# Kernel tuning notes

Hardware: AMD Instinct MI355X
Metric: run time of the kernel (lower is better)

## Reference

```python
import jax, jax.numpy as jnp
import numpy as np

N = 50000   # num_entities
F = 300     # node feature dim
D = 128     # embedding_dim
H = 4       # heads
C = D // H  # per-head out channels (32)
E = 640000  # num edges
R = 200     # num_relations
L = 2       # num_layers
NEG_SLOPE = 0.2  # PyG GATv2Conv default


def setup_inputs() -> dict:
    key = jax.random.key(0)
    ks = jax.random.split(key, 14)
    s = 0.1
    return {
        "entity": jnp.arange(N, dtype=jnp.int32),
        "edge_index": jax.random.randint(ks[0], (2, E), 0, N, dtype=jnp.int32),
        "edge_type": jax.random.randint(ks[1], (E,), 0, R, dtype=jnp.int32),
        # learned parameters
        "node_features": jax.random.normal(ks[2], (N, F), jnp.float32) * s,   # entity_embedding table
        "rel_emb": jax.random.normal(ks[3], (R, D), jnp.float32) * s,          # relation_embedding
        "proj_w": jax.random.normal(ks[4], (F, D), jnp.float32) * s,           # project Linear
        "proj_b": jnp.zeros((D,), jnp.float32),
        # per-layer GATv2Conv params, stacked over L layers
        "w_l": jax.random.normal(ks[5], (L, D, H * C), jnp.float32) * s,       # lin_l weight
        "b_l": jnp.zeros((L, H * C), jnp.float32),
        "w_r": jax.random.normal(ks[6], (L, D, H * C), jnp.float32) * s,       # lin_r weight
        "b_r": jnp.zeros((L, H * C), jnp.float32),
        "w_e": jax.random.normal(ks[7], (L, D, H * C), jnp.float32) * s,       # lin_edge weight (no bias)
        "att": jax.random.normal(ks[8], (L, H, C), jnp.float32) * s,           # attention vector a
        "bias": jnp.zeros((L, H * C), jnp.float32),                             # output bias
    }


def _gatv2_layer(x, src, dst, edge_attr, w_l, b_l, w_r, b_r, w_e, att, bias):
    # x: [N, D], edge_attr: [E, D]
    x_l = (x @ w_l + b_l).reshape(N, H, C)
    x_r = (x @ w_r + b_r).reshape(N, H, C)
    e = (edge_attr @ w_e).reshape(E, H, C)
    # per-edge message (gather src/dst + edge), GATv2: leaky_relu BEFORE attention dot
    m = jax.nn.leaky_relu(x_l[src] + x_r[dst] + e, NEG_SLOPE)   # [E, H, C]
    logits = jnp.einsum('ehc,hc->eh', m, att)                    # [E, H]
    # segment softmax over edges grouped by destination node
    lmax = jax.ops.segment_max(logits, dst, num_segments=N)      # [N, H]
    ex = jnp.exp(logits - lmax[dst])                             # [E, H]
    denom = jax.ops.segment_sum(ex, dst, num_segments=N)         # [N, H]
    alpha = ex / denom[dst]                                      # [E, H]
    # scatter-aggregate messages x_l[src] weighted by alpha
    out = jax.ops.segment_sum(x_l[src] * alpha[:, :, None], dst, num_segments=N)  # [N, H, C]
    return out.reshape(N, H * C) + bias


def reference(entity, edge_index, edge_type, node_features, rel_emb,
              proj_w, proj_b, w_l, b_l, w_r, b_r, w_e, att, bias):
    x = node_features[entity]            # embedding lookup
    x = x @ proj_w + proj_b              # project to D
    edge_attr = rel_emb[edge_type]       # [E, D] (weights=False -> no edge_weight scaling)
    src, dst = edge_index[0], edge_index[1]
    for i in range(L):
        x = _gatv2_layer(x, src, dst, edge_attr,
                         w_l[i], b_l[i], w_r[i], b_r[i], w_e[i], att[i], bias[i])
        if i != L - 1:
            x = jax.nn.elu(x)            # dropout inactive (eval mode)
    return x
```

## Files before the change

kernel.cpp:

```cpp
#include <hip/hip_runtime.h>

#define NN 50000
#define FF 300
#define DD 128
#define HH 4
#define CC 32
#define EE 640000
#define RR 200
#define LL 2
#define SB ((NN + 255) / 256)
#define PK 320
#define WTOT (128 * PK + 4 * 128 * 128)
#define HB ((EE + 255) / 256)
#define WB ((WTOT + 255) / 256)
#define RB (LL * RR / 2)

typedef unsigned short u16;
typedef unsigned int u32;
typedef _Float16 h2   __attribute__((ext_vector_type(2)));
typedef _Float16 half8 __attribute__((ext_vector_type(8)));
typedef __attribute__((ext_vector_type(4))) float floatx4;

__device__ __forceinline__ u16 f2h(float f) {
    union { _Float16 h; u16 u; } v; v.h = (_Float16)f; return v.u;
}
__device__ __forceinline__ float h2f(u16 u) {
    union { u16 u; _Float16 h; } v; v.u = u; return (float)v.h;
}
__device__ __forceinline__ h2 u2h2(u32 p) {
    union { u32 u; h2 h; } v; v.u = p; return v.h;
}
__device__ __forceinline__ h2 hmax2(h2 a, h2 b) {
#if __has_builtin(__builtin_elementwise_max)
    return __builtin_elementwise_max(a, b);
#else
    h2 r; r.x = a.x > b.x ? a.x : b.x; r.y = a.y > b.y ? a.y : b.y; return r;
#endif
}
__device__ __forceinline__ float hdot2(h2 a, h2 b, float c) {
#if __has_builtin(__builtin_amdgcn_fdot2)
    return __builtin_amdgcn_fdot2(a, b, c, false);
#else
    return c + (float)a.x * (float)b.x + (float)a.y * (float)b.y;
#endif
}

__device__ __forceinline__ int block_excl_scan(int v, int* lds4, int* total) {
    int lane = threadIdx.x & 63, wid = threadIdx.x >> 6;
    int x = v;
    #pragma unroll
    for (int off = 1; off < 64; off <<= 1) {
        int y = __shfl_up(x, off, 64);
        if (lane >= off) x += y;
    }
    if (lane == 63) lds4[wid] = x;
    __syncthreads();
    int add = 0;
    #pragma unroll
    for (int w = 0; w < 4; w++) add += (w < wid) ? lds4[w] : 0;
    *total = lds4[0] + lds4[1] + lds4[2] + lds4[3];
    return x + add - v;
}

__global__ __launch_bounds__(256)
void prep_kernel(const int* __restrict__ ei, int* __restrict__ counts,
                 const float* __restrict__ proj_w, const float* __restrict__ w_l,
                 const float* __restrict__ w_r, u16* __restrict__ wt,
                 const float* __restrict__ rel_emb, const float* __restrict__ w_e,
                 u16* __restrict__ erel)
{
    __shared__ float rv[2][DD];
    int b = blockIdx.x, tid = threadIdx.x;
    if (b < HB) {
        int e = b * 256 + tid;
        if (e < EE) atomicAdd(&counts[ei[EE + e]], 1);
    } else if (b < HB + WB) {
        int i = (b - HB) * 256 + tid;
        if (i < WTOT) {
            float v;
            if (i < 128 * PK) {
                int n = i / PK, k = i - n * PK;
                v = (k < FF) ? proj_w[(size_t)k * DD + n] : 0.f;
            } else {
                int j = i - 128 * PK;
                int seg = j >> 14;
                int r = j & 16383;
                int n = r >> 7, k = r & 127;
                const float* src = (seg < 2) ? (w_l + (size_t)seg * DD * DD)
                                             : (w_r + (size_t)(seg - 2) * DD * DD);
                v = src[(size_t)k * DD + n];
            }
            wt[i] = f2h(v);
        }
    } else {
        int half = tid >> 7, d = tid & 127;
        int lr = (b - HB - WB) * 2 + half;
        int l = lr / RR, r = lr - l * RR;
        rv[half][d] = rel_emb[r * DD + d];
        __syncthreads();
        const float* W = w_e + (size_t)l * DD * DD;
        float acc = 0.f;
        #pragma unroll 8
        for (int k = 0; k < DD; k++) acc += rv[half][k] * W[k * DD + d];
        erel[(size_t)lr * DD + d] = f2h(acc);
    }
}

template<bool AF16, bool GATHER>
__global__ __launch_bounds__(256)
void gemm_mfma_kernel(const void* __restrict__ A_, const int* __restrict__ rowidx,
                      int lda, int K, int Ka, int ldb,
                      const u16* __restrict__ BT1, const float* __restrict__ bias1,
                      u16* __restrict__ C1,
                      const u16* __restrict__ BT2, const float* __restrict__ bias2,
                      u16* __restrict__ C2, int M)
{
    const u16*   BT   = (blockIdx.y == 0) ? BT1 : BT2;
    const float* bias = (blockIdx.y == 0) ? bias1 : bias2;
    u16*         Cout = (blockIdx.y == 0) ? C1 : C2;

    __shared__ u16 As[128][72];
    __shared__ u16 Bs[128][72];
    int tid  = threadIdx.x;
    int m0   = blockIdx.x * 128;
    int wave = tid >> 6, lane = tid & 63;
    int quad = lane >> 4, l16 = lane & 15;
    int wrow = (wave >> 1) * 64, wcol = (wave & 1) * 64;

    floatx4 acc[4][4];
    #pragma unroll
    for (int i = 0; i < 4; i++)
        #pragma unroll
        for (int j = 0; j < 4; j++) acc[i][j] = (floatx4){0.f, 0.f, 0.f, 0.f};

    int ar = tid >> 1, ah = tid & 1;
    int arow = m0 + ar;
    int rid = (arow < M) ? (GATHER ? rowidx[arow] : arow) : 0;

    for (int kk = 0; kk < K; kk += 64) {
        #pragma unroll
        for (int q = 0; q < 2; q++) {
            int kb = kk + ah * 32 + q * 16;
            u16 tmp[16];
            if (AF16) {
                const u16* Ap = (const u16*)A_ + (size_t)rid * lda + kb;
                if (kb + 16 <= Ka) {
                    *(half8*)&tmp[0] = *(const half8*)Ap;
                    *(half8*)&tmp[8] = *(const half8*)(Ap + 8);
                } else {
                    #pragma unroll
                    for (int j = 0; j < 16; j++) tmp[j] = (kb + j < Ka) ? Ap[j] : (u16)0;
                }
            } else {
                const float* Ap = (const float*)A_ + (size_t)rid * lda + kb;
                if (kb + 16 <= Ka) {
                    #pragma unroll
                    for (int qq = 0; qq < 4; qq++) {
                        float4 f = *(const float4*)(Ap + qq * 4);
                        tmp[qq*4+0] = f2h(f.x); tmp[qq*4+1] = f2h(f.y);
                        tmp[qq*4+2] = f2h(f.z); tmp[qq*4+3] = f2h(f.w);
                    }
                } else {
                    #pragma unroll
                    for (int j = 0; j < 16; j++) tmp[j] = (kb + j < Ka) ? f2h(Ap[j]) : (u16)0;
                }
            }
            *(half8*)&As[ar][ah * 32 + q * 16]     = *(half8*)&tmp[0];
            *(half8*)&As[ar][ah * 32 + q * 16 + 8] = *(half8*)&tmp[8];
        }
        {
            const u16* Bp = BT + (size_t)ar * ldb + kk + ah * 32;
            #pragma unroll
            for (int q = 0; q < 4; q++)
                *(half8*)&Bs[ar][ah * 32 + q * 8] = *(const half8*)(Bp + q * 8);
        }
        __syncthreads();
        #pragma unroll
        for (int ks = 0; ks < 2; ks++) {
            half8 af[4], bfr[4];
            #pragma unroll
            for (int i = 0; i < 4; i++)
                af[i] = *(const half8*)&As[wrow + i * 16 + l16][ks * 32 + quad * 8];
            #pragma unroll
            for (int j = 0; j < 4; j++)
                bfr[j] = *(const half8*)&Bs[wcol + j * 16 + l16][ks * 32 + quad * 8];
            #pragma unroll
            for (int i = 0; i < 4; i++)
                #pragma unroll
                for (int j = 0; j < 4; j++)
                    acc[i][j] = __builtin_amdgcn_mfma_f32_16x16x32_f16(
                        af[i], bfr[j], acc[i][j], 0, 0, 0);
        }
        __syncthreads();
    }

    #pragma unroll
    for (int i = 0; i < 4; i++) {
        #pragma unroll
        for (int rr = 0; rr < 4; rr++) {
            int row = m0 + wrow + i * 16 + quad * 4 + rr;
            if (row < M) {
                #pragma unroll
                for (int j = 0; j < 4; j++) {
                    int col = wcol + j * 16 + l16;
                    Cout[(size_t)row * DD + col] = f2h(acc[i][j][rr] + bias[col]);
                }
            }
        }
    }
}

__global__ __launch_bounds__(256)
void scan_local_kernel(const int* __restrict__ counts, int* __restrict__ offsets,
                       int* __restrict__ bsum)
{
    __shared__ int lds4[4];
    int i = blockIdx.x * 256 + threadIdx.x;
    int v = (i < NN) ? counts[i] : 0;
    int total;
    int ex = block_excl_scan(v, lds4, &total);
    if (i < NN) offsets[i] = ex;
    if (threadIdx.x == 0) bsum[blockIdx.x] = total;
}

__global__ __launch_bounds__(256)
void scan_bsum_kernel(int* __restrict__ bsum)
{
    __shared__ int lds4[4];
    int t = threadIdx.x;
    int v = (t < SB) ? bsum[t] : 0;
    int total;
    int ex = block_excl_scan(v, lds4, &total);
    if (t < SB) bsum[t] = ex;
}

__global__ __launch_bounds__(256)
void scatter_kernel(const int* __restrict__ ei, const int* __restrict__ et,
                    const int* __restrict__ offsets, const int* __restrict__ bsum,
                    int* __restrict__ fill, u32* __restrict__ dstorder)
{
    int e = blockIdx.x * 256 + threadIdx.x;
    if (e >= EE) return;
    int d = ei[EE + e];
    int pos = offsets[d] + bsum[d >> 8] + atomicAdd(&fill[d], 1);
    dstorder[pos] = (u32)ei[e] | ((u32)et[e] << 16);
}

__global__ __launch_bounds__(256)
void node_kernel(const u32* __restrict__ dstorder, const int* __restrict__ offsets,
                 const int* __restrict__ bsum,
                 const u16* __restrict__ xl, const u16* __restrict__ xr,
                 const u16* __restrict__ erel, const float* __restrict__ att,
                 const float* __restrict__ bias,
                 u16* __restrict__ xnext, float* __restrict__ outp, int is_last)
{
    int tid  = threadIdx.x;
    int node = blockIdx.x * 4 + (tid >> 6);
    int lane = tid & 63;
    if (node >= NN) return;
    int g  = lane >> 4;
    int gl = lane & 15;
    int c0 = gl * 8;
    int beg = offsets[node] + bsum[node >> 8];
    int end = (node == NN - 1) ? EE : offsets[node + 1] + bsum[(node + 1) >> 8];

    h2 xrh[4], atth[4];
    {
        const u32* xp = (const u32*)&xr[(size_t)node * DD + c0];
        #pragma unroll
        for (int q = 0; q < 4; q++) xrh[q] = u2h2(xp[q]);
        #pragma unroll
        for (int q = 0; q < 4; q++) {
            float2 av = *(const float2*)&att[c0 + q * 2];
            atth[q] = (h2){(_Float16)av.x, (_Float16)av.y};
        }
    }
    const h2 c02 = (h2){(_Float16)0.2f, (_Float16)0.2f};

    float s = 0.f;
    h2 a2[4];
    #pragma unroll
    for (int q = 0; q < 4; q++) a2[q] = (h2){(_Float16)0.f, (_Float16)0.f};

    for (int base = beg; base < end; base += 4) {
        int es = base + g;
        bool valid = es < end;
        u32 st = valid ? dstorder[es] : 0;
        int src = st & 0xffff;
        int typ = st >> 16;
        const u32* xp = (const u32*)&xl[(size_t)src * DD + c0];
        const u32* ep = (const u32*)&erel[(size_t)typ * DD + c0];
        h2 xh[4];
        float p = 0.f;
        #pragma unroll
        for (int q = 0; q < 4; q++) {
            xh[q] = u2h2(xp[q]);
            h2 m = (xh[q] + xrh[q]) + u2h2(ep[q]);
            m = hmax2(m, m * c02);
            p = hdot2(m, atth[q], p);
        }
        p += __shfl_xor(p, 1, 64);
        p += __shfl_xor(p, 2, 64);
        float w = valid ? __expf(fminf(p, 60.f)) : 0.f;
        s += w;
        h2 wh = (h2){(_Float16)w, (_Float16)w};
        #pragma unroll
        for (int q = 0; q < 4; q++) a2[q] += wh * xh[q];
    }

    float a[8];
    #pragma unroll
    for (int q = 0; q < 4; q++) { a[q*2] = (float)a2[q].x; a[q*2+1] = (float)a2[q].y; }
    #pragma unroll
    for (int j = 0; j < 8; j++) {
        a[j] += __shfl_xor(a[j], 16, 64);
        a[j] += __shfl_xor(a[j], 32, 64);
    }
    s += __shfl_xor(s, 16, 64);
    s += __shfl_xor(s, 32, 64);

    if (lane < 16) {
        float rh = 1.f / fmaxf(s, 1e-30f);
        float4 b0 = *(const float4*)&bias[c0];
        float4 b1 = *(const float4*)&bias[c0 + 4];
        float bv[8] = {b0.x, b0.y, b0.z, b0.w, b1.x, b1.y, b1.z, b1.w};
        float v[8];
        #pragma unroll
        for (int j = 0; j < 8; j++) v[j] = a[j] * rh + bv[j];
        if (is_last) {
            float4* op = (float4*)&outp[(size_t)node * DD + c0];
            op[0] = make_float4(v[0], v[1], v[2], v[3]);
            op[1] = make_float4(v[4], v[5], v[6], v[7]);
        } else {
            u16 pk[8];
            #pragma unroll
            for (int j = 0; j < 8; j++) {
                float w2 = v[j] > 0.f ? v[j] : __expf(v[j]) - 1.f;
                pk[j] = f2h(w2);
            }
            *(half8*)&xnext[(size_t)node * DD + c0] = *(half8*)pk;
        }
    }
}

extern "C" void kernel_launch(void* const* d_in, const int* in_sizes, int n_in,
                              void* d_out, int out_size, void* d_ws, size_t ws_size,
                              hipStream_t stream)
{
    const int*   entity        = (const int*)d_in[0];
    const int*   edge_index    = (const int*)d_in[1];
    const int*   edge_type     = (const int*)d_in[2];
    const float* node_features = (const float*)d_in[3];
    const float* rel_emb       = (const float*)d_in[4];
    const float* proj_w        = (const float*)d_in[5];
    const float* proj_b        = (const float*)d_in[6];
    const float* w_l           = (const float*)d_in[7];
    const float* b_l           = (const float*)d_in[8];
    const float* w_r           = (const float*)d_in[9];
    const float* b_r           = (const float*)d_in[10];
    const float* w_e           = (const float*)d_in[11];
    const float* att           = (const float*)d_in[12];
    const float* bias          = (const float*)d_in[13];

    u16*   xb      = (u16*)d_ws;
    u16*   xl      = xb + (size_t)NN * DD;
    u16*   xr      = xl + (size_t)NN * DD;
    u16*   erel    = xr + (size_t)NN * DD;
    u16*   wt      = erel + (size_t)LL * RR * DD;
    u32*   dstorder= (u32*)(wt + WTOT);
    int*   counts  = (int*)(dstorder + (size_t)EE);
    int*   fill    = counts + NN;
    int*   offsets = fill + NN;
    int*   bsum    = offsets + NN;

    hipMemsetAsync(counts, 0, (size_t)NN * 2 * sizeof(int), stream);
    prep_kernel<<<HB + WB + RB, 256, 0, stream>>>(
        edge_index, counts, proj_w, w_l, w_r, wt, rel_emb, w_e, erel);

    scan_local_kernel<<<SB, 256, 0, stream>>>(counts, offsets, bsum);
    scan_bsum_kernel<<<1, 256, 0, stream>>>(bsum);
    scatter_kernel<<<(EE + 255) / 256, 256, 0, stream>>>(
        edge_index, edge_type, offsets, bsum, fill, dstorder);

    const u16* wtProj = wt;
    const int GB = (NN + 127) / 128;
    gemm_mfma_kernel<false, true><<<dim3(GB, 1), 256, 0, stream>>>(
        node_features, entity, FF, PK, FF, PK,
        wtProj, proj_b, xb, wtProj, proj_b, xb, NN);

    for (int l = 0; l < LL; l++) {
        const u16* wtl = wt + 128 * PK + l * 16384;
        const u16* wtr = wt + 128 * PK + 32768 + l * 16384;
        gemm_mfma_kernel<true, false><<<dim3(GB, 2), 256, 0, stream>>>(
            xb, nullptr, DD, DD, DD, DD,
            wtl, b_l + l * DD, xl,
            wtr, b_r + l * DD, xr, NN);

        node_kernel<<<(NN + 3) / 4, 256, 0, stream>>>(
            dstorder, offsets, bsum, xl, xr, erel + (size_t)l * RR * DD,
            att + (size_t)l * DD, bias + (size_t)l * DD,
            xb, (float*)d_out, l == LL - 1);
    }
}
```

Before: 333.1 us.

## Fold projection into layer-0 weights, fuse dual GEMM, prefetch edges in node kernel

Layer-0 lin_l and lin_r are folded into the input projection by precomputing proj_w@w_l and proj_w@w_r, plus the matching fused biases, in the prep kernel. This removes one whole GEMM pass and the fp16 intermediate x. The GEMM now computes both outputs from a single 64-row A tile with a 256-column B tile, so A is read once instead of twice. The node kernel now uses 8 lanes per edge with 16 channels each, handles 8 edges per iteration, and software-prefetches the next edge's gathers. The risks are more fp16 rounding from the folded weights and extra registers in the node kernel.

```diff
diff --git a/kernel.cpp b/kernel.cpp
--- a/kernel.cpp
+++ b/kernel.cpp
@@ -10,9 +10,11 @@
 #define LL 2
 #define SB ((NN + 255) / 256)
 #define PK 320
-#define WTOT (128 * PK + 4 * 128 * 128)
+#define WCONV (2 * 128 * 128)
+#define WTOT (2 * 128 * PK + WCONV)
 #define HB ((EE + 255) / 256)
-#define WB ((WTOT + 255) / 256)
+#define WB (WCONV / 256)
+#define FB PK
 #define RB (LL * RR / 2)
 
 typedef unsigned short u16;
@@ -67,7 +69,9 @@
                  const float* __restrict__ proj_w, const float* __restrict__ w_l,
                  const float* __restrict__ w_r, u16* __restrict__ wt,
                  const float* __restrict__ rel_emb, const float* __restrict__ w_e,
-                 u16* __restrict__ erel)
+                 u16* __restrict__ erel, const float* __restrict__ proj_b,
+                 const float* __restrict__ b_l, const float* __restrict__ b_r,
+                 float* __restrict__ fbias)
 {
     __shared__ float rv[2][DD];
     int b = blockIdx.x, tid = threadIdx.x;
@@ -76,25 +80,36 @@
         if (e < EE) atomicAdd(&counts[ei[EE + e]], 1);
     } else if (b < HB + WB) {
         int i = (b - HB) * 256 + tid;
-        if (i < WTOT) {
-            float v;
-            if (i < 128 * PK) {
-                int n = i / PK, k = i - n * PK;
-                v = (k < FF) ? proj_w[(size_t)k * DD + n] : 0.f;
-            } else {
-                int j = i - 128 * PK;
-                int seg = j >> 14;
-                int r = j & 16383;
-                int n = r >> 7, k = r & 127;
-                const float* src = (seg < 2) ? (w_l + (size_t)seg * DD * DD)
-                                             : (w_r + (size_t)(seg - 2) * DD * DD);
-                v = src[(size_t)k * DD + n];
-            }
-            wt[i] = f2h(v);
-        }
+        int seg = i >> 14;
+        int r = i & 16383;
+        int n = r >> 7, k = r & 127;
+        const float* src = (seg == 0 ? w_l : w_r) + (size_t)DD * DD;
+        wt[2 * 128 * PK + i] = f2h(src[(size_t)k * DD + n]);
+    } else if (b < HB + WB + FB) {
+        int half = tid >> 7, d = tid & 127;
+        int pp = (b - HB - WB) * 2 + half;
+        int lr = pp / PK, k = pp - lr * PK;
+        rv[half][d] = (k < FF) ? proj_w[(size_t)k * DD + d] : 0.f;
+        __syncthreads();
+        float acc = 0.f;
+        if (k < FF) {
+            const float* W = lr ? w_r : w_l;
+            #pragma unroll 8
+            for (int j = 0; j < DD; j++) acc += rv[half][j] * W[(size_t)j * DD + d];
+        }
+        wt[(size_t)lr * 128 * PK + (size_t)d * PK + k] = f2h(acc);
+    } else if (b == HB + WB + FB) {
+        int half = tid >> 7, d = tid & 127;
+        if (tid < DD) rv[0][tid] = proj_b[tid];
+        __syncthreads();
+        const float* W = half ? w_r : w_l;
+        float acc = half ? b_r[d] : b_l[d];
+        #pragma unroll 8
+        for (int j = 0; j < DD; j++) acc += rv[0][j] * W[(size_t)j * DD + d];
+        fbias[half * DD + d] = acc;
     } else {
         int half = tid >> 7, d = tid & 127;
-        int lr = (b - HB - WB) * 2 + half;
+        int lr = (b - HB - WB - FB - 1) * 2 + half;
         int l = lr / RR, r = lr - l * RR;
         rv[half][d] = rel_emb[r * DD + d];
         __syncthreads();
@@ -108,24 +123,20 @@
 
 template<bool AF16, bool GATHER>
 __global__ __launch_bounds__(256)
-void gemm_mfma_kernel(const void* __restrict__ A_, const int* __restrict__ rowidx,
+void gemm_dual_kernel(const void* __restrict__ A_, const int* __restrict__ rowidx,
                       int lda, int K, int Ka, int ldb,
                       const u16* __restrict__ BT1, const float* __restrict__ bias1,
                       u16* __restrict__ C1,
                       const u16* __restrict__ BT2, const float* __restrict__ bias2,
                       u16* __restrict__ C2, int M)
 {
-    const u16*   BT   = (blockIdx.y == 0) ? BT1 : BT2;
-    const float* bias = (blockIdx.y == 0) ? bias1 : bias2;
-    u16*         Cout = (blockIdx.y == 0) ? C1 : C2;
-
-    __shared__ u16 As[128][72];
-    __shared__ u16 Bs[128][72];
+    __shared__ u16 As[64][72];
+    __shared__ u16 Bs[256][72];
     int tid  = threadIdx.x;
-    int m0   = blockIdx.x * 128;
+    int m0   = blockIdx.x * 64;
     int wave = tid >> 6, lane = tid & 63;
     int quad = lane >> 4, l16 = lane & 15;
-    int wrow = (wave >> 1) * 64, wcol = (wave & 1) * 64;
+    int wcol = wave * 64;
 
     floatx4 acc[4][4];
     #pragma unroll
@@ -133,77 +144,76 @@
         #pragma unroll
         for (int j = 0; j < 4; j++) acc[i][j] = (floatx4){0.f, 0.f, 0.f, 0.f};
 
-    int ar = tid >> 1, ah = tid & 1;
+    int ar = tid >> 2, ak = (tid & 3) * 16;
     int arow = m0 + ar;
     int rid = (arow < M) ? (GATHER ? rowidx[arow] : arow) : 0;
+    const u16* Brow = (tid < 128) ? (BT1 + (size_t)tid * ldb)
+                                  : (BT2 + (size_t)(tid - 128) * ldb);
 
     for (int kk = 0; kk < K; kk += 64) {
-        #pragma unroll
-        for (int q = 0; q < 2; q++) {
-            int kb = kk + ah * 32 + q * 16;
-            u16 tmp[16];
-            if (AF16) {
-                const u16* Ap = (const u16*)A_ + (size_t)rid * lda + kb;
-                if (kb + 16 <= Ka) {
-                    *(half8*)&tmp[0] = *(const half8*)Ap;
-                    *(half8*)&tmp[8] = *(const half8*)(Ap + 8);
-                } else {
-                    #pragma unroll
-                    for (int j = 0; j < 16; j++) tmp[j] = (kb + j < Ka) ? Ap[j] : (u16)0;
+        int kb = kk + ak;
+        u16 tmp[16];
+        if (AF16) {
+            const u16* Ap = (const u16*)A_ + (size_t)rid * lda + kb;
+            if (kb + 16 <= Ka) {
+                *(half8*)&tmp[0] = *(const half8*)Ap;
+                *(half8*)&tmp[8] = *(const half8*)(Ap + 8);
+            } else {
+                #pragma unroll
+                for (int j = 0; j < 16; j++) tmp[j] = (kb + j < Ka) ? Ap[j] : (u16)0;
+            }
+        } else {
+            const float* Ap = (const float*)A_ + (size_t)rid * lda + kb;
+            if (kb + 16 <= Ka) {
+                #pragma unroll
+                for (int qq = 0; qq < 4; qq++) {
+                    float4 f = *(const float4*)(Ap + qq * 4);
+                    tmp[qq*4+0] = f2h(f.x); tmp[qq*4+1] = f2h(f.y);
+                    tmp[qq*4+2] = f2h(f.z); tmp[qq*4+3] = f2h(f.w);
                 }
             } else {
-                const float* Ap = (const float*)A_ + (size_t)rid * lda + kb;
-                if (kb + 16 <= Ka) {
-                    #pragma unroll
-                    for (int qq = 0; qq < 4; qq++) {
-                        float4 f = *(const float4*)(Ap + qq * 4);
-                        tmp[qq*4+0] = f2h(f.x); tmp[qq*4+1] = f2h(f.y);
-                        tmp[qq*4+2] = f2h(f.z); tmp[qq*4+3] = f2h(f.w);
-                    }
-                } else {
-                    #pragma unroll
-                    for (int j = 0; j < 16; j++) tmp[j] = (kb + j < Ka) ? f2h(Ap[j]) : (u16)0;
-                }
+                #pragma unroll
+                for (int j = 0; j < 16; j++) tmp[j] = (kb + j < Ka) ? f2h(Ap[j]) : (u16)0;
             }
-            *(half8*)&As[ar][ah * 32 + q * 16]     = *(half8*)&tmp[0];
-            *(half8*)&As[ar][ah * 32 + q * 16 + 8] = *(half8*)&tmp[8];
-        }
-        {
-            const u16* Bp = BT + (size_t)ar * ldb + kk + ah * 32;
-            #pragma unroll
-            for (int q = 0; q < 4; q++)
-                *(half8*)&Bs[ar][ah * 32 + q * 8] = *(const half8*)(Bp + q * 8);
-        }
+        }
+        *(half8*)&As[ar][ak]     = *(half8*)&tmp[0];
+        *(half8*)&As[ar][ak + 8] = *(half8*)&tmp[8];
+        #pragma unroll
+        for (int q = 0; q < 8; q++)
+            *(half8*)&Bs[tid][q * 8] = *(const half8*)(Brow + kk + q * 8);
         __syncthreads();
         #pragma unroll
         for (int ks = 0; ks < 2; ks++) {
-            half8 af[4], bfr[4];
+            half8 af[4], bf[4];
             #pragma unroll
             for (int i = 0; i < 4; i++)
-                af[i] = *(const half8*)&As[wrow + i * 16 + l16][ks * 32 + quad * 8];
+                af[i] = *(const half8*)&As[i * 16 + l16][ks * 32 + quad * 8];
             #pragma unroll
             for (int j = 0; j < 4; j++)
-                bfr[j] = *(const half8*)&Bs[wcol + j * 16 + l16][ks * 32 + quad * 8];
+                bf[j] = *(const half8*)&Bs[wcol + j * 16 + l16][ks * 32 + quad * 8];
             #pragma unroll
             for (int i = 0; i < 4; i++)
                 #pragma unroll
                 for (int j = 0; j < 4; j++)
                     acc[i][j] = __builtin_amdgcn_mfma_f32_16x16x32_f16(
-                        af[i], bfr[j], acc[i][j], 0, 0, 0);
+                        af[i], bf[j], acc[i][j], 0, 0, 0);
         }
         __syncthreads();
     }
 
+    u16* Cw = (wave < 2) ? C1 : C2;
+    const float* bw = (wave < 2) ? bias1 : bias2;
+    int cbase = wcol & 127;
     #pragma unroll
     for (int i = 0; i < 4; i++) {
         #pragma unroll
         for (int rr = 0; rr < 4; rr++) {
-            int row = m0 + wrow + i * 16 + quad * 4 + rr;
+            int row = m0 + i * 16 + quad * 4 + rr;
             if (row < M) {
                 #pragma unroll
                 for (int j = 0; j < 4; j++) {
-                    int col = wcol + j * 16 + l16;
-                    Cout[(size_t)row * DD + col] = f2h(acc[i][j][rr] + bias[col]);
+                    int col = cbase + j * 16 + l16;
+                    Cw[(size_t)row * DD + col] = f2h(acc[i][j][rr] + bw[col]);
                 }
             }
         }
@@ -258,19 +268,19 @@
     int node = blockIdx.x * 4 + (tid >> 6);
     int lane = tid & 63;
     if (node >= NN) return;
-    int g  = lane >> 4;
-    int gl = lane & 15;
-    int c0 = gl * 8;
+    int g  = lane >> 3;
+    int gl = lane & 7;
+    int c0 = gl * 16;
     int beg = offsets[node] + bsum[node >> 8];
     int end = (node == NN - 1) ? EE : offsets[node + 1] + bsum[(node + 1) >> 8];
 
-    h2 xrh[4], atth[4];
+    h2 xrh[8], atth[8];
     {
         const u32* xp = (const u32*)&xr[(size_t)node * DD + c0];
         #pragma unroll
-        for (int q = 0; q < 4; q++) xrh[q] = u2h2(xp[q]);
-        #pragma unroll
-        for (int q = 0; q < 4; q++) {
+        for (int q = 0; q < 8; q++) xrh[q] = u2h2(xp[q]);
+        #pragma unroll
+        for (int q = 0; q < 8; q++) {
             float2 av = *(const float2*)&att[c0 + q * 2];
             atth[q] = (h2){(_Float16)av.x, (_Float16)av.y};
         }
@@ -278,67 +288,89 @@
     const h2 c02 = (h2){(_Float16)0.2f, (_Float16)0.2f};
 
     float s = 0.f;
-    h2 a2[4];
-    #pragma unroll
-    for (int q = 0; q < 4; q++) a2[q] = (h2){(_Float16)0.f, (_Float16)0.f};
-
-    for (int base = beg; base < end; base += 4) {
-        int es = base + g;
-        bool valid = es < end;
-        u32 st = valid ? dstorder[es] : 0;
-        int src = st & 0xffff;
-        int typ = st >> 16;
+    h2 a2[8];
+    #pragma unroll
+    for (int q = 0; q < 8; q++) a2[q] = (h2){(_Float16)0.f, (_Float16)0.f};
+
+    int es = beg + g;
+    u32 stB = (es + 8 < end) ? dstorder[es + 8] : 0u;
+    h2 xhA[8], ehA[8];
+    {
+        u32 stA = (es < end) ? dstorder[es] : 0u;
+        int src = stA & 0xffff, typ = stA >> 16;
         const u32* xp = (const u32*)&xl[(size_t)src * DD + c0];
         const u32* ep = (const u32*)&erel[(size_t)typ * DD + c0];
-        h2 xh[4];
+        #pragma unroll
+        for (int q = 0; q < 8; q++) { xhA[q] = u2h2(xp[q]); ehA[q] = u2h2(ep[q]); }
+    }
+
+    for (int base = beg; base < end; base += 8) {
+        u32 stN = (base + 16 + g < end) ? dstorder[base + 16 + g] : 0u;
+        h2 xhB[8], ehB[8];
+        {
+            int src = stB & 0xffff, typ = stB >> 16;
+            const u32* xp = (const u32*)&xl[(size_t)src * DD + c0];
+            const u32* ep = (const u32*)&erel[(size_t)typ * DD + c0];
+            #pragma unroll
+            for (int q = 0; q < 8; q++) { xhB[q] = u2h2(xp[q]); ehB[q] = u2h2(ep[q]); }
+        }
         float p = 0.f;
         #pragma unroll
-        for (int q = 0; q < 4; q++) {
-            xh[q] = u2h2(xp[q]);
-            h2 m = (xh[q] + xrh[q]) + u2h2(ep[q]);
+        for (int q = 0; q < 8; q++) {
+            h2 m = (xhA[q] + xrh[q]) + ehA[q];
             m = hmax2(m, m * c02);
             p = hdot2(m, atth[q], p);
         }
         p += __shfl_xor(p, 1, 64);
-        p += __shfl_xor(p, 2, 64);
+        bool valid = (base + g) < end;
         float w = valid ? __expf(fminf(p, 60.f)) : 0.f;
         s += w;
         h2 wh = (h2){(_Float16)w, (_Float16)w};
         #pragma unroll
-        for (int q = 0; q < 4; q++) a2[q] += wh * xh[q];
-    }
-
-    float a[8];
-    #pragma unroll
-    for (int q = 0; q < 4; q++) { a[q*2] = (float)a2[q].x; a[q*2+1] = (float)a2[q].y; }
-    #pragma unroll
-    for (int j = 0; j < 8; j++) {
+        for (int q = 0; q < 8; q++) a2[q] += wh * xhA[q];
+        #pragma unroll
+        for (int q = 0; q < 8; q++) { xhA[q] = xhB[q]; ehA[q] = ehB[q]; }
+        stB = stN;
+    }
+
+    float a[16];
+    #pragma unroll
+    for (int q = 0; q < 8; q++) { a[q*2] = (float)a2[q].x; a[q*2+1] = (float)a2[q].y; }
+    #pragma unroll
+    for (int j = 0; j < 16; j++) {
+        a[j] += __shfl_xor(a[j], 8, 64);
         a[j] += __shfl_xor(a[j], 16, 64);
         a[j] += __shfl_xor(a[j], 32, 64);
     }
+    s += __shfl_xor(s, 8, 64);
     s += __shfl_xor(s, 16, 64);
     s += __shfl_xor(s, 32, 64);
 
-    if (lane < 16) {
+    if (lane < 8) {
+        int cc = lane * 16;
         float rh = 1.f / fmaxf(s, 1e-30f);
-        float4 b0 = *(const float4*)&bias[c0];
-        float4 b1 = *(const float4*)&bias[c0 + 4];
-        float bv[8] = {b0.x, b0.y, b0.z, b0.w, b1.x, b1.y, b1.z, b1.w};
-        float v[8];
-        #pragma unroll
-        for (int j = 0; j < 8; j++) v[j] = a[j] * rh + bv[j];
+        float bv[16], v[16];
+        #pragma unroll
+        for (int qq = 0; qq < 4; qq++) {
+            float4 bq = *(const float4*)&bias[cc + qq * 4];
+            bv[qq*4+0] = bq.x; bv[qq*4+1] = bq.y; bv[qq*4+2] = bq.z; bv[qq*4+3] = bq.w;
+        }
+        #pragma unroll
+        for (int j = 0; j < 16; j++) v[j] = a[j] * rh + bv[j];
         if (is_last) {
-            float4* op = (float4*)&outp[(size_t)node * DD + c0];
-            op[0] = make_float4(v[0], v[1], v[2], v[3]);
-            op[1] = make_float4(v[4], v[5], v[6], v[7]);
+            float4* op = (float4*)&outp[(size_t)node * DD + cc];
+            #pragma unroll
+            for (int qq = 0; qq < 4; qq++)
+                op[qq] = make_float4(v[qq*4+0], v[qq*4+1], v[qq*4+2], v[qq*4+3]);
         } else {
-            u16 pk[8];
-            #pragma unroll
-            for (int j = 0; j < 8; j++) {
+            u16 pk[16];
+            #pragma unroll
+            for (int j = 0; j < 16; j++) {
                 float w2 = v[j] > 0.f ? v[j] : __expf(v[j]) - 1.f;
                 pk[j] = f2h(w2);
             }
-            *(half8*)&xnext[(size_t)node * DD + c0] = *(half8*)pk;
+            *(half8*)&xnext[(size_t)node * DD + cc]     = *(half8*)&pk[0];
+            *(half8*)&xnext[(size_t)node * DD + cc + 8] = *(half8*)&pk[8];
         }
     }
 }
@@ -372,33 +404,33 @@
     int*   fill    = counts + NN;
     int*   offsets = fill + NN;
     int*   bsum    = offsets + NN;
+    float* fbias   = (float*)(bsum + SB);
 
     hipMemsetAsync(counts, 0, (size_t)NN * 2 * sizeof(int), stream);
-    prep_kernel<<<HB + WB + RB, 256, 0, stream>>>(
-        edge_index, counts, proj_w, w_l, w_r, wt, rel_emb, w_e, erel);
+    prep_kernel<<<HB + WB + FB + 1 + RB, 256, 0, stream>>>(
+        edge_index, counts, proj_w, w_l, w_r, wt, rel_emb, w_e, erel,
+        proj_b, b_l, b_r, fbias);
 
     scan_local_kernel<<<SB, 256, 0, stream>>>(counts, offsets, bsum);
     scan_bsum_kernel<<<1, 256, 0, stream>>>(bsum);
     scatter_kernel<<<(EE + 255) / 256, 256, 0, stream>>>(
         edge_index, edge_type, offsets, bsum, fill, dstorder);
 
-    const u16* wtProj = wt;
-    const int GB = (NN + 127) / 128;
-    gemm_mfma_kernel<false, true><<<dim3(GB, 1), 256, 0, stream>>>(
+    const int GB2 = (NN + 63) / 64;
+
+    gemm_dual_kernel<false, true><<<GB2, 256, 0, stream>>>(
         node_features, entity, FF, PK, FF, PK,
-        wtProj, proj_b, xb, wtProj, proj_b, xb, NN);
-
-    for (int l = 0; l < LL; l++) {
-        const u16* wtl = wt + 128 * PK + l * 16384;
-        const u16* wtr = wt + 128 * PK + 32768 + l * 16384;
-        gemm_mfma_kernel<true, false><<<dim3(GB, 2), 256, 0, stream>>>(
-            xb, nullptr, DD, DD, DD, DD,
-            wtl, b_l + l * DD, xl,
-            wtr, b_r + l * DD, xr, NN);
-
-        node_kernel<<<(NN + 3) / 4, 256, 0, stream>>>(
-            dstorder, offsets, bsum, xl, xr, erel + (size_t)l * RR * DD,
-            att + (size_t)l * DD, bias + (size_t)l * DD,
-            xb, (float*)d_out, l == LL - 1);
-    }
-}
+        wt, fbias, xl,
+        wt + (size_t)128 * PK, fbias + DD, xr, NN);
+    node_kernel<<<(NN + 3) / 4, 256, 0, stream>>>(
+        dstorder, offsets, bsum, xl, xr, erel,
+        att, bias, xb, (float*)d_out, 0);
+
+    gemm_dual_kernel<true, false><<<GB2, 256, 0, stream>>>(
+        xb, nullptr, DD, DD, DD, DD,
+        wt + (size_t)2 * 128 * PK, b_l + DD, xl,
+        wt + (size_t)2 * 128 * PK + 128 * 128, b_r + DD, xr, NN);
+    node_kernel<<<(NN + 3) / 4, 256, 0, stream>>>(
+        dstorder, offsets, bsum, xl, xr, erel + (size_t)RR * DD,
+        att + DD, bias + DD, xb, (float*)d_out, 1);
+}
```

After: 346.8 us. +4.1%, slower.
